# Optimization experiments

Hardware: AMD Instinct MI355X
Metric: run time of the kernel (lower is better)

Reference implementation:

```python
import jax, jax.numpy as jnp
import numpy as np

N, E, B = 50000, 800000, 64
IN_DIM, HID = 128, 64
H1 = 2  # heads in gat1
NEG_SLOPE = 0.2


def _glorot(key, shape):
    fan_in = shape[0]
    return jax.random.normal(key, shape, dtype=jnp.float32) / jnp.sqrt(jnp.float32(fan_in))


def setup_inputs() -> dict:
    key = jax.random.key(0)
    ks = jax.random.split(key, 24)
    x = jax.random.normal(ks[0], (N, IN_DIM), dtype=jnp.float32)
    edge_index = jax.random.randint(ks[1], (2, E), 0, N, dtype=jnp.int64)
    batch = jnp.sort(jax.random.randint(ks[2], (N,), 0, B, dtype=jnp.int64))
    d = {
        'x': x, 'edge_index': edge_index, 'batch': batch,
        # gat1: in=128 -> heads=2, out=64 (concat -> 128)
        'w1_l': _glorot(ks[3], (IN_DIM, H1 * HID)), 'b1_l': jnp.zeros((H1 * HID,), jnp.float32),
        'w1_r': _glorot(ks[4], (IN_DIM, H1 * HID)), 'b1_r': jnp.zeros((H1 * HID,), jnp.float32),
        'att1': _glorot(ks[5], (H1, HID)), 'bias1': jnp.zeros((H1 * HID,), jnp.float32),
        # gat2: in=128 -> heads=1, out=64
        'w2_l': _glorot(ks[6], (H1 * HID, HID)), 'b2_l': jnp.zeros((HID,), jnp.float32),
        'w2_r': _glorot(ks[7], (H1 * HID, HID)), 'b2_r': jnp.zeros((HID,), jnp.float32),
        'att2': _glorot(ks[8], (1, HID)), 'bias2': jnp.zeros((HID,), jnp.float32),
        # gate_nn: Linear(64,64) -> ReLU -> Linear(64,1)
        'gate_w1': _glorot(ks[9], (HID, HID)), 'gate_b1': jnp.zeros((HID,), jnp.float32),
        'gate_w2': _glorot(ks[10], (HID, 1)), 'gate_b2': jnp.zeros((1,), jnp.float32),
        # MLP head
        'lin1_w': _glorot(ks[11], (HID, HID)), 'lin1_b': jnp.zeros((HID,), jnp.float32),
        'lin2_w': _glorot(ks[12], (HID, 1)), 'lin2_b': jnp.zeros((1,), jnp.float32),
    }
    return d


def _segment_softmax(scores, seg, num_segments):
    # scores: [E, H]; softmax over edges sharing the same seg id (per column)
    m = jax.ops.segment_max(scores, seg, num_segments=num_segments)
    m = jnp.where(jnp.isfinite(m), m, 0.0)
    ex = jnp.exp(scores - m[seg])
    s = jax.ops.segment_sum(ex, seg, num_segments=num_segments)
    return ex / (s[seg] + 1e-16)


def _gatv2(x, src, dst, w_l, b_l, w_r, b_r, att, bias, heads, out_dim, n_nodes):
    xl = (x @ w_l + b_l).reshape(n_nodes, heads, out_dim)
    xr = (x @ w_r + b_r).reshape(n_nodes, heads, out_dim)
    e = jax.nn.leaky_relu(xl[src] + xr[dst], NEG_SLOPE)      # [E,H,D]
    score = jnp.einsum('ehd,hd->eh', e, att)                  # [E,H]
    alpha = _segment_softmax(score, dst, n_nodes)             # [E,H]
    out = jax.ops.segment_sum(alpha[..., None] * xl[src], dst, num_segments=n_nodes)
    return out.reshape(n_nodes, heads * out_dim) + bias


def reference(x, edge_index, batch, w1_l, b1_l, w1_r, b1_r, att1, bias1,
              w2_l, b2_l, w2_r, b2_r, att2, bias2,
              gate_w1, gate_b1, gate_w2, gate_b2,
              lin1_w, lin1_b, lin2_w, lin2_b):
    n = x.shape[0]
    # PyG GATv2Conv default add_self_loops=True
    loop = jnp.arange(n, dtype=edge_index.dtype)
    src = jnp.concatenate([edge_index[0], loop])
    dst = jnp.concatenate([edge_index[1], loop])

    h = jax.nn.relu(_gatv2(x, src, dst, w1_l, b1_l, w1_r, b1_r, att1, bias1, H1, HID, n))
    h = jax.nn.relu(_gatv2(h, src, dst, w2_l, b2_l, w2_r, b2_r, att2, bias2, 1, HID, n))

    # GlobalAttention pool: gate = gate_nn(h); softmax over batch; weighted sum
    gate = jax.nn.relu(h @ gate_w1 + gate_b1) @ gate_w2 + gate_b2     # [N,1]
    alpha = _segment_softmax(gate, batch, B)                           # [N,1]
    pooled = jax.ops.segment_sum(alpha * h, batch, num_segments=B)     # [B,HID]

    out = jax.nn.relu(pooled @ lin1_w + lin1_b)
    out = (out @ lin2_w + lin2_b).squeeze(-1)                          # [B]
    return out
```

## Files before the change

### kernel.cpp

```cpp
#include <hip/hip_runtime.h>

typedef float v2f __attribute__((ext_vector_type(2)));
typedef float v4f __attribute__((ext_vector_type(4)));
typedef _Float16 h4 __attribute__((ext_vector_type(4)));

template<int N> struct IC { static constexpr int value = N; };


__global__ void k_init(const float* __restrict__ w1_l, const float* __restrict__ w1_r,
                       const float* __restrict__ b1_l, const float* __restrict__ b1_r,
                       const float* __restrict__ w2_l, const float* __restrict__ w2_r,
                       const float* __restrict__ b2_l, const float* __restrict__ b2_r,
                       float* __restrict__ wc1, float* __restrict__ bc1,
                       float* __restrict__ wc2, float* __restrict__ bc2,
                       int* __restrict__ deg, int n){
  int i = blockIdx.x*256 + threadIdx.x;
  if (i < n) deg[i] = 0;
  if (i < 128*256){
    int k = i >> 8, j = i & 255;
    wc1[i] = (j < 128) ? w1_l[k*128 + j] : w1_r[k*128 + (j - 128)];
  }
  if (i < 128*128){
    int k = i >> 7, j = i & 127;
    wc2[i] = (j < 64) ? w2_l[k*64 + j] : w2_r[k*64 + (j - 64)];
  }
  if (i < 256) bc1[i] = (i < 128) ? b1_l[i] : b1_r[i - 128];
  if (i < 128) bc2[i] = (i < 64)  ? b2_l[i] : b2_r[i - 64];
}

__global__ void k_hist(const int* __restrict__ dstp, int* __restrict__ deg, int E){
  int e = blockIdx.x*256 + threadIdx.x;
  if (e < E) atomicAdd(&deg[dstp[e]], 1);
}

__global__ void k_scan1(const int* __restrict__ deg, int* __restrict__ rowptr,
                        int* __restrict__ bsum, int n){
  __shared__ int s[256];
  int i = blockIdx.x*256 + threadIdx.x;
  int v = (i < n) ? deg[i] + 1 : 0;
  s[threadIdx.x] = v;
  __syncthreads();
  for (int off = 1; off < 256; off <<= 1){
    int t = (threadIdx.x >= off) ? s[threadIdx.x - off] : 0;
    __syncthreads();
    s[threadIdx.x] += t;
    __syncthreads();
  }
  if (i < n) rowptr[i] = s[threadIdx.x] - v;
  if (threadIdx.x == 255) bsum[blockIdx.x] = s[255];
}

__global__ void k_scan2(int* bsum, int nb){
  __shared__ int s[256];
  int v = (threadIdx.x < nb) ? bsum[threadIdx.x] : 0;
  s[threadIdx.x] = v;
  __syncthreads();
  for (int off = 1; off < 256; off <<= 1){
    int t = (threadIdx.x >= off) ? s[threadIdx.x - off] : 0;
    __syncthreads();
    s[threadIdx.x] += t;
    __syncthreads();
  }
  if (threadIdx.x < nb) bsum[threadIdx.x] = s[threadIdx.x] - v;
}

__global__ void k_scan3(int* rowptr, const int* __restrict__ bsum,
                        int* __restrict__ srcs, int* __restrict__ cursor,
                        int n, int total){
  int i = blockIdx.x*256 + threadIdx.x;
  if (i < n){
    int b = rowptr[i] + bsum[blockIdx.x];
    rowptr[i] = b;
    srcs[b] = i;
    cursor[i] = b + 1;
  }
  if (i == 0) rowptr[n] = total;
}

__global__ void k_scatter(const int* __restrict__ srcp, const int* __restrict__ dstp,
                          int* __restrict__ cursor, int* __restrict__ srcs, int E){
  int e = blockIdx.x*256 + threadIdx.x;
  if (e < E){
    int p = atomicAdd(&cursor[dstp[e]], 1);
    srcs[p] = srcp[e];
  }
}


#define TBM 64
#define TBN 128
#define TBK 32

__global__ __launch_bounds__(256, 4) void k_gemm64(
    const float* __restrict__ A, const float* __restrict__ W,
    const float* __restrict__ bias, _Float16* __restrict__ Cxl,
    float* __restrict__ Cxr, int M, int K, int N, int xlCols){
  __shared__ float As[TBK][TBM];
  __shared__ float Ws[TBK][TBN];
  int bm = blockIdx.x * TBM, bn = blockIdx.y * TBN;
  int tid = threadIdx.x;
  int tx = tid & 15, ty = tid >> 4;
  float acc[4][8] = {};
  for (int k0 = 0; k0 < K; k0 += TBK){
    #pragma unroll
    for (int l = 0; l < 2; l++){
      int idx = tid + l*256;
      int r = idx >> 3, kq = (idx & 7) * 4;
      float4 v = make_float4(0.f, 0.f, 0.f, 0.f);
      if (bm + r < M) v = *(const float4*)(A + (size_t)(bm + r)*K + k0 + kq);
      int rc = r ^ ((idx & 7) << 3);
      As[kq+0][rc] = v.x; As[kq+1][rc] = v.y; As[kq+2][rc] = v.z; As[kq+3][rc] = v.w;
    }
    #pragma unroll
    for (int l = 0; l < 4; l++){
      int idx = tid + l*256;
      int kr = idx >> 5, wc = (idx & 31) * 4;
      *(float4*)(&Ws[kr][wc]) = *(const float4*)(W + (size_t)(k0 + kr)*N + bn + wc);
    }
    __syncthreads();
    #pragma unroll
    for (int k = 0; k < TBK; k++){
      float a[4], w[8];
      *(float4*)(a)   = *(const float4*)(&As[k][(ty*4) ^ (((k >> 2) & 7) << 3)]);
      *(float4*)(w)   = *(const float4*)(&Ws[k][tx*4]);
      *(float4*)(w+4) = *(const float4*)(&Ws[k][64 + tx*4]);
      #pragma unroll
      for (int i = 0; i < 4; i++)
        #pragma unroll
        for (int j = 0; j < 8; j++)
          acc[i][j] = fmaf(a[i], w[j], acc[i][j]);
    }
    __syncthreads();
  }
  int NR = N - xlCols;
  #pragma unroll
  for (int i = 0; i < 4; i++){
    int r = bm + ty*4 + i;
    if (r < M){
      #pragma unroll
      for (int g = 0; g < 2; g++){
        int c = bn + g*64 + tx*4;
        float o0 = acc[i][g*4+0] + bias[c+0];
        float o1 = acc[i][g*4+1] + bias[c+1];
        float o2 = acc[i][g*4+2] + bias[c+2];
        float o3 = acc[i][g*4+3] + bias[c+3];
        if (c < xlCols){
          h4 oh = {(_Float16)o0, (_Float16)o1, (_Float16)o2, (_Float16)o3};
          *(h4*)(Cxl + (size_t)r*xlCols + c) = oh;
        } else {
          float4 of = make_float4(o0, o1, o2, o3);
          *(float4*)(Cxr + (size_t)r*NR + (c - xlCols)) = of;
        }
      }
    }
  }
}


template<int CTRL>
__device__ __forceinline__ float dpp_add(float x){
  int t = __builtin_amdgcn_update_dpp(0, __float_as_int(x), CTRL, 0xf, 0xf, true);
  return x + __int_as_float(t);
}


template<int H>
__global__ __launch_bounds__(256) void k_gat_fused(
    const _Float16* __restrict__ xlh, const float* __restrict__ xr,
    const int* __restrict__ rowptr, const int* __restrict__ srcs,
    const float* __restrict__ att, const float* __restrict__ bias,
    float* __restrict__ out, int n){
  int gid = blockIdx.x * blockDim.x + threadIdx.x;
  int nd = gid >> 6, lane = gid & 63;
  if (nd >= n) return;
  constexpr int SHIFTB = (H == 2) ? 8 : 7;
  constexpr int EPI = (H == 2) ? 2 : 4;
  const int q = lane & 15;
  const int hsel = (H == 2) ? ((lane >> 4) & 1) : 0;
  const int elane = (H == 2) ? (lane >> 5) : (lane >> 4);
  const int fpos = hsel*64 + q*4;
  const unsigned foff = (unsigned)fpos * 2u;
  const char* __restrict__ xbase = (const char*)xlh;
  v4f xrv = *(const v4f*)(xr + (size_t)nd*(H*64) + fpos);
  v4f av  = *(const v4f*)(att + fpos);
  v4f acc = {0.f, 0.f, 0.f, 0.f};
  float den = 0.f;
  int s0 = rowptr[nd], s1 = rowptr[nd+1];
  for (int base = s0; base < s1; base += 64){
    int idx = base + lane;
    int sv = (idx < s1) ? srcs[idx] : 0;
    int cnt = min(64, s1 - base);
    auto batchU = [&](int i, auto Uc, bool full){
      constexpr int U = decltype(Uc)::value;
      int aidx[U];
      h4 hv[U];
      #pragma unroll
      for (int u = 0; u < U; u++)
        aidx[u] = __builtin_amdgcn_ds_bpermute((i + u*EPI + elane) << 2, sv);
      #pragma unroll
      for (int u = 0; u < U; u++)
        hv[u] = *(const h4*)(xbase + (((unsigned)aidx[u] << SHIFTB) + foff));
      #pragma unroll
      for (int u = 0; u < U; u++){
        v4f xv = {(float)hv[u].x, (float)hv[u].y, (float)hv[u].z, (float)hv[u].w};
        v4f t  = xv + xrv;
        v4f lt = __builtin_elementwise_max(t, t * 0.2f);
        v4f pr = lt * av;
        float p = (pr.x + pr.y) + (pr.z + pr.w);
        p = dpp_add<0x111>(p);
        p = dpp_add<0x112>(p);
        p = dpp_add<0x114>(p);
        p = dpp_add<0x118>(p);
        p = __int_as_float(__builtin_amdgcn_ds_swizzle(__float_as_int(p), 0x1F0));
        float ex = __expf(p);
        if (!full) ex = (elane < cnt - (i + u*EPI)) ? ex : 0.f;
        den += ex;
        acc += xv * ex;
      }
    };
    int i = 0;
    for (; i + 8*EPI <= cnt; i += 8*EPI) batchU(i, IC<8>{}, true);
    if (i + 4*EPI <= cnt){ batchU(i, IC<4>{}, true); i += 4*EPI; }
    if (i + 2*EPI <= cnt){ batchU(i, IC<2>{}, true); i += 2*EPI; }
    for (; i < cnt; i += EPI) batchU(i, IC<1>{}, i + EPI <= cnt);
  }
  if (H == 1){
    den   += __shfl_xor(den,   16, 64);
    acc.x += __shfl_xor(acc.x, 16, 64);
    acc.y += __shfl_xor(acc.y, 16, 64);
    acc.z += __shfl_xor(acc.z, 16, 64);
    acc.w += __shfl_xor(acc.w, 16, 64);
  }
  den   += __shfl_xor(den,   32, 64);
  acc.x += __shfl_xor(acc.x, 32, 64);
  acc.y += __shfl_xor(acc.y, 32, 64);
  acc.z += __shfl_xor(acc.z, 32, 64);
  acc.w += __shfl_xor(acc.w, 32, 64);
  if (lane < 16*H){
    v4f bv = *(const v4f*)(bias + lane*4);
    float inv = 1.f / (den + 1e-16f);
    v4f o = acc * inv + bv;
    v4f z = {0.f, 0.f, 0.f, 0.f};
    o = __builtin_elementwise_max(o, z);
    *(v4f*)(out + (size_t)nd*(H*64) + lane*4) = o;
  }
}


__global__ __launch_bounds__(256) void k_gate(
    const float* __restrict__ h2, const float* __restrict__ gw1,
    const float* __restrict__ gb1, const float* __restrict__ gw2,
    const float* __restrict__ gb2, float* __restrict__ exn, int M){
  __shared__ float As[32][64 + 4];
  __shared__ float Ws[32][64];
  int bm = blockIdx.x * 64;
  int tid = threadIdx.x;
  int tx = tid & 15, ty = tid >> 4;
  float acc[4][4] = {};
  for (int k0 = 0; k0 < 64; k0 += 32){
    #pragma unroll
    for (int l = 0; l < 2; l++){
      int idx = tid + l*256;
      int r = idx >> 3, c4 = (idx & 7) * 4;
      float4 v = make_float4(0.f, 0.f, 0.f, 0.f);
      if (bm + r < M) v = *(const float4*)(h2 + (size_t)(bm + r)*64 + k0 + c4);
      As[c4+0][r] = v.x; As[c4+1][r] = v.y; As[c4+2][r] = v.z; As[c4+3][r] = v.w;
      int kr = idx >> 4, wc4 = (idx & 15) * 4;
      *(float4*)(&Ws[kr][wc4]) = *(const float4*)(gw1 + (size_t)(k0 + kr)*64 + wc4);
    }
    __syncthreads();
    #pragma unroll
    for (int k = 0; k < 32; k++){
      float4 a4 = *(const float4*)(&As[k][ty*4]);
      float4 w4 = *(const float4*)(&Ws[k][tx*4]);
      float av[4] = {a4.x, a4.y, a4.z, a4.w};
      float wv[4] = {w4.x, w4.y, w4.z, w4.w};
      #pragma unroll
      for (int i = 0; i < 4; i++)
        #pragma unroll
        for (int j = 0; j < 4; j++)
          acc[i][j] = fmaf(av[i], wv[j], acc[i][j]);
    }
    __syncthreads();
  }
  float4 b4 = *(const float4*)(gb1 + tx*4);
  float4 w2 = *(const float4*)(gw2 + tx*4);
  float gb2v = gb2[0];
  #pragma unroll
  for (int i = 0; i < 4; i++){
    float p = fmaxf(acc[i][0] + b4.x, 0.f) * w2.x;
    p = fmaf(fmaxf(acc[i][1] + b4.y, 0.f), w2.y, p);
    p = fmaf(fmaxf(acc[i][2] + b4.z, 0.f), w2.z, p);
    p = fmaf(fmaxf(acc[i][3] + b4.w, 0.f), w2.w, p);
    p = dpp_add<0x111>(p);
    p = dpp_add<0x112>(p);
    p = dpp_add<0x114>(p);
    p = dpp_add<0x118>(p);
    if (tx == 15){
      int r = bm + ty*4 + i;
      if (r < M) exn[r] = __expf(p + gb2v);
    }
  }
}


__global__ __launch_bounds__(1024) void k_pool_mlp(
    const float* __restrict__ h2, const float* __restrict__ exn,
    const int* __restrict__ batch, int n,
    const float* __restrict__ l1w, const float* __restrict__ l1b,
    const float* __restrict__ l2w, const float* __restrict__ l2b,
    float* __restrict__ out){
  __shared__ float accs[16][64];
  __shared__ float dens[16];
  int b = blockIdx.x;
  int tid = threadIdx.x, lane = tid & 63, wv = tid >> 6;
  int lo = 0, hi = n;
  while (lo < hi){ int m = (lo + hi) >> 1; if (batch[m] < b) lo = m + 1; else hi = m; }
  int start = lo;
  hi = n;
  while (lo < hi){ int m = (lo + hi) >> 1; if (batch[m] < b + 1) lo = m + 1; else hi = m; }
  int end = lo;
  float acc = 0.f, den = 0.f;
  for (int nd = start + wv; nd < end; nd += 16){
    float ex = exn[nd];
    den += ex;
    acc = fmaf(ex, h2[(size_t)nd*64 + lane], acc);
  }
  accs[wv][lane] = acc;
  if (lane == 0) dens[wv] = den;
  __syncthreads();
  if (wv == 0){
    float p = 0.f, d = 0.f;
    #pragma unroll
    for (int w = 0; w < 16; w++){ p += accs[w][lane]; d += dens[w]; }
    p = p / (d + 1e-16f);
    float t = l1b[lane];
    #pragma unroll
    for (int k = 0; k < 64; k++)
      t = fmaf(__shfl(p, k, 64), l1w[k*64 + lane], t);
    t = fmaxf(t, 0.f) * l2w[lane];
    #pragma unroll
    for (int off = 32; off; off >>= 1) t += __shfl_xor(t, off, 64);
    if (lane == 0) out[b] = t + l2b[0];
  }
}


extern "C" void kernel_launch(void* const* d_in, const int* in_sizes, int n_in,
                              void* d_out, int out_size, void* d_ws, size_t ws_size,
                              hipStream_t stream){
  const float* x    = (const float*)d_in[0];
  const int*   ei   = (const int*)  d_in[1];
  const int*   batch= (const int*)  d_in[2];
  const float* w1_l = (const float*)d_in[3];  const float* b1_l = (const float*)d_in[4];
  const float* w1_r = (const float*)d_in[5];  const float* b1_r = (const float*)d_in[6];
  const float* att1 = (const float*)d_in[7];  const float* bias1= (const float*)d_in[8];
  const float* w2_l = (const float*)d_in[9];  const float* b2_l = (const float*)d_in[10];
  const float* w2_r = (const float*)d_in[11]; const float* b2_r = (const float*)d_in[12];
  const float* att2 = (const float*)d_in[13]; const float* bias2= (const float*)d_in[14];
  const float* gw1  = (const float*)d_in[15]; const float* gb1  = (const float*)d_in[16];
  const float* gw2  = (const float*)d_in[17]; const float* gb2  = (const float*)d_in[18];
  const float* l1w  = (const float*)d_in[19]; const float* l1b  = (const float*)d_in[20];
  const float* l2w  = (const float*)d_in[21]; const float* l2b  = (const float*)d_in[22];

  const int n = in_sizes[0] / 128;
  const int E = in_sizes[1] / 2;
  const int Bb = out_size;
  const int Etot = E + n;
  const int* srcp = ei;
  const int* dstp = ei + E;

  char* wsbase = (char*)d_ws;
  size_t off = 0;
  auto alloc = [&](size_t bytes)->char*{
    char* p = wsbase + off;
    off = (off + bytes + 255) & ~(size_t)255;
    return p;
  };
  int*   deg    = (int*)  alloc((size_t)n*4);
  int*   rowptr = (int*)  alloc((size_t)(n+1)*4);
  int*   cursor = (int*)  alloc((size_t)n*4);
  int*   bsum   = (int*)  alloc(1024);
  int*   srcs   = (int*)  alloc((size_t)Etot*4);
  float* wc1    = (float*)alloc(128*256*4);
  float* bc1    = (float*)alloc(256*4);
  float* wc2    = (float*)alloc(128*128*4);
  float* bc2    = (float*)alloc(128*4);
  _Float16* xlh1 = (_Float16*)alloc((size_t)n*128*2);
  float* xr1    = (float*)alloc((size_t)n*128*4);
  float* h1     = (float*)alloc((size_t)n*128*4);
  _Float16* xlh2 = xlh1;
  float* xr2 = xr1;
  float* h2  = xr1 + (size_t)n*64;
  float* exn = h1;

  int nb = (n + 255) / 256;
  int eb = (E + 255) / 256;
  int ib = (((n > 32768) ? n : 32768) + 255) / 256;

  k_init<<<ib, 256, 0, stream>>>(w1_l, w1_r, b1_l, b1_r, w2_l, w2_r, b2_l, b2_r,
                                 wc1, bc1, wc2, bc2, deg, n);
  k_hist<<<eb, 256, 0, stream>>>(dstp, deg, E);
  k_scan1<<<nb, 256, 0, stream>>>(deg, rowptr, bsum, n);
  k_scan2<<<1, 256, 0, stream>>>(bsum, nb);
  k_scan3<<<nb, 256, 0, stream>>>(rowptr, bsum, srcs, cursor, n, Etot);
  k_scatter<<<eb, 256, 0, stream>>>(srcp, dstp, cursor, srcs, E);

  dim3 g1((n + TBM - 1)/TBM, 256/TBN);
  k_gemm64<<<g1, 256, 0, stream>>>(x, wc1, bc1, xlh1, xr1, n, 128, 256, 128);
  long long thr = (long long)n * 64;
  int gatb = (int)((thr + 255)/256);
  k_gat_fused<2><<<gatb, 256, 0, stream>>>(xlh1, xr1, rowptr, srcs, att1, bias1, h1, n);

  dim3 g2((n + TBM - 1)/TBM, 128/TBN);
  k_gemm64<<<g2, 256, 0, stream>>>(h1, wc2, bc2, xlh2, xr2, n, 128, 128, 64);
  k_gat_fused<1><<<gatb, 256, 0, stream>>>(xlh2, xr2, rowptr, srcs, att2, bias2, h2, n);

  k_gate<<<(n + 63)/64, 256, 0, stream>>>(h2, gw1, gb1, gw2, gb2, exn, n);

  k_pool_mlp<<<Bb, 1024, 0, stream>>>(h2, exn, batch, n, l1w, l1b, l2w, l2b, (float*)d_out);
}
```

Measured before the change: 372.2 us.

## Replace FP32 SIMT GEMMs with split-FP16 MFMA GEMM

Swaps the scalar FMA GEMM used for both GAT linear projections for one built on matrix-core instructions. Operands are split into high and low FP16 parts and combined with three MFMA products to stay close to FP32 accuracy. Weights are pre-split and transposed in the init kernel, and A is converted to FP16 while it is staged in LDS. The aim is to cut the GEMM's ALU cost, at the price of extra conversion work and scalar (non-vectorised) output stores.

```diff
diff --git a/kernel.cpp b/kernel.cpp
--- a/kernel.cpp
+++ b/kernel.cpp
@@ -3,6 +3,7 @@
 typedef float v2f __attribute__((ext_vector_type(2)));
 typedef float v4f __attribute__((ext_vector_type(4)));
 typedef _Float16 h4 __attribute__((ext_vector_type(4)));
+typedef _Float16 f16x8 __attribute__((ext_vector_type(8)));
 
 template<int N> struct IC { static constexpr int value = N; };
 
@@ -11,18 +12,23 @@
                        const float* __restrict__ b1_l, const float* __restrict__ b1_r,
                        const float* __restrict__ w2_l, const float* __restrict__ w2_r,
                        const float* __restrict__ b2_l, const float* __restrict__ b2_r,
-                       float* __restrict__ wc1, float* __restrict__ bc1,
-                       float* __restrict__ wc2, float* __restrict__ bc2,
+                       _Float16* __restrict__ wc1h, _Float16* __restrict__ wc1l,
+                       _Float16* __restrict__ wc2h, _Float16* __restrict__ wc2l,
+                       float* __restrict__ bc1, float* __restrict__ bc2,
                        int* __restrict__ deg, int n){
   int i = blockIdx.x*256 + threadIdx.x;
   if (i < n) deg[i] = 0;
-  if (i < 128*256){
-    int k = i >> 8, j = i & 255;
-    wc1[i] = (j < 128) ? w1_l[k*128 + j] : w1_r[k*128 + (j - 128)];
+  if (i < 256*128){
+    int col = i >> 7, k = i & 127;
+    float v = (col < 128) ? w1_l[k*128 + col] : w1_r[k*128 + (col - 128)];
+    _Float16 h = (_Float16)v;
+    wc1h[i] = h; wc1l[i] = (_Float16)(v - (float)h);
   }
   if (i < 128*128){
-    int k = i >> 7, j = i & 127;
-    wc2[i] = (j < 64) ? w2_l[k*64 + j] : w2_r[k*64 + (j - 64)];
+    int col = i >> 7, k = i & 127;
+    float v = (col < 64) ? w2_l[k*64 + col] : w2_r[k*64 + (col - 64)];
+    _Float16 h = (_Float16)v;
+    wc2h[i] = h; wc2l[i] = (_Float16)(v - (float)h);
   }
   if (i < 256) bc1[i] = (i < 128) ? b1_l[i] : b1_r[i - 128];
   if (i < 128) bc2[i] = (i < 64)  ? b2_l[i] : b2_r[i - 64];
@@ -87,70 +93,79 @@
 }
 
 
-#define TBM 64
-#define TBN 128
-#define TBK 32
-
-__global__ __launch_bounds__(256, 4) void k_gemm64(
-    const float* __restrict__ A, const float* __restrict__ W,
-    const float* __restrict__ bias, _Float16* __restrict__ Cxl,
-    float* __restrict__ Cxr, int M, int K, int N, int xlCols){
-  __shared__ float As[TBK][TBM];
-  __shared__ float Ws[TBK][TBN];
-  int bm = blockIdx.x * TBM, bn = blockIdx.y * TBN;
+#define MBM 64
+#define MBN 128
+#define MBK 32
+
+__device__ __forceinline__ int lds_idx(int row, int k){
+  return row*32 + ((((k >> 3) ^ row) & 3) << 3) + (k & 7);
+}
+
+__global__ __launch_bounds__(256) void k_gemm_mfma(
+    const float* __restrict__ A, const _Float16* __restrict__ Wh,
+    const _Float16* __restrict__ Wl, const float* __restrict__ bias,
+    _Float16* __restrict__ Cxl, float* __restrict__ Cxr,
+    int M, int K, int N, int xlCols){
+  __shared__ _Float16 Ah[MBM*MBK], Al[MBM*MBK];
+  __shared__ _Float16 Bh[MBN*MBK], Bl[MBN*MBK];
+  int bm = blockIdx.x * MBM, bn = blockIdx.y * MBN;
   int tid = threadIdx.x;
-  int tx = tid & 15, ty = tid >> 4;
-  float acc[4][8] = {};
-  for (int k0 = 0; k0 < K; k0 += TBK){
+  int lane = tid & 63, wv = tid >> 6;
+  v4f acc[8] = {};
+  const int fragoff = (lane & 15)*32 + ((((lane >> 4) ^ lane) & 3) << 3);
+  for (int k0 = 0; k0 < K; k0 += MBK){
     #pragma unroll
     for (int l = 0; l < 2; l++){
       int idx = tid + l*256;
       int r = idx >> 3, kq = (idx & 7) * 4;
       float4 v = make_float4(0.f, 0.f, 0.f, 0.f);
       if (bm + r < M) v = *(const float4*)(A + (size_t)(bm + r)*K + k0 + kq);
-      int rc = r ^ ((idx & 7) << 3);
-      As[kq+0][rc] = v.x; As[kq+1][rc] = v.y; As[kq+2][rc] = v.z; As[kq+3][rc] = v.w;
-    }
-    #pragma unroll
-    for (int l = 0; l < 4; l++){
+      _Float16 e0 = (_Float16)v.x, e1 = (_Float16)v.y,
+               e2 = (_Float16)v.z, e3 = (_Float16)v.w;
+      h4 hh = {e0, e1, e2, e3};
+      h4 ll = {(_Float16)(v.x - (float)e0), (_Float16)(v.y - (float)e1),
+               (_Float16)(v.z - (float)e2), (_Float16)(v.w - (float)e3)};
+      int o = lds_idx(r, kq);
+      *(h4*)(&Ah[o]) = hh;
+      *(h4*)(&Al[o]) = ll;
+    }
+    #pragma unroll
+    for (int l = 0; l < 2; l++){
       int idx = tid + l*256;
-      int kr = idx >> 5, wc = (idx & 31) * 4;
-      *(float4*)(&Ws[kr][wc]) = *(const float4*)(W + (size_t)(k0 + kr)*N + bn + wc);
-    }
-    __syncthreads();
-    #pragma unroll
-    for (int k = 0; k < TBK; k++){
-      float a[4], w[8];
-      *(float4*)(a)   = *(const float4*)(&As[k][(ty*4) ^ (((k >> 2) & 7) << 3)]);
-      *(float4*)(w)   = *(const float4*)(&Ws[k][tx*4]);
-      *(float4*)(w+4) = *(const float4*)(&Ws[k][64 + tx*4]);
-      #pragma unroll
-      for (int i = 0; i < 4; i++)
-        #pragma unroll
-        for (int j = 0; j < 8; j++)
-          acc[i][j] = fmaf(a[i], w[j], acc[i][j]);
-    }
-    __syncthreads();
-  }
+      int c = idx >> 2, kc = (idx & 3) * 8;
+      size_t go = (size_t)(bn + c)*K + k0 + kc;
+      int o = lds_idx(c, kc);
+      *(f16x8*)(&Bh[o]) = *(const f16x8*)(Wh + go);
+      *(f16x8*)(&Bl[o]) = *(const f16x8*)(Wl + go);
+    }
+    __syncthreads();
+    f16x8 ah = *(const f16x8*)(&Ah[wv*16*32 + fragoff]);
+    f16x8 al = *(const f16x8*)(&Al[wv*16*32 + fragoff]);
+    #pragma unroll
+    for (int t = 0; t < 8; t++){
+      f16x8 bh = *(const f16x8*)(&Bh[t*16*32 + fragoff]);
+      f16x8 bl = *(const f16x8*)(&Bl[t*16*32 + fragoff]);
+      acc[t] = __builtin_amdgcn_mfma_f32_16x16x32_f16(ah, bh, acc[t], 0, 0, 0);
+      acc[t] = __builtin_amdgcn_mfma_f32_16x16x32_f16(ah, bl, acc[t], 0, 0, 0);
+      acc[t] = __builtin_amdgcn_mfma_f32_16x16x32_f16(al, bh, acc[t], 0, 0, 0);
+    }
+    __syncthreads();
+  }
+  int rbase = bm + wv*16 + (lane >> 4)*4;
+  int cl = lane & 15;
   int NR = N - xlCols;
   #pragma unroll
-  for (int i = 0; i < 4; i++){
-    int r = bm + ty*4 + i;
-    if (r < M){
-      #pragma unroll
-      for (int g = 0; g < 2; g++){
-        int c = bn + g*64 + tx*4;
-        float o0 = acc[i][g*4+0] + bias[c+0];
-        float o1 = acc[i][g*4+1] + bias[c+1];
-        float o2 = acc[i][g*4+2] + bias[c+2];
-        float o3 = acc[i][g*4+3] + bias[c+3];
-        if (c < xlCols){
-          h4 oh = {(_Float16)o0, (_Float16)o1, (_Float16)o2, (_Float16)o3};
-          *(h4*)(Cxl + (size_t)r*xlCols + c) = oh;
-        } else {
-          float4 of = make_float4(o0, o1, o2, o3);
-          *(float4*)(Cxr + (size_t)r*NR + (c - xlCols)) = of;
-        }
+  for (int t = 0; t < 8; t++){
+    int col = bn + t*16 + cl;
+    float bv = bias[col];
+    bool isXl = (bn + t*16) < xlCols;
+    #pragma unroll
+    for (int i = 0; i < 4; i++){
+      int r = rbase + i;
+      if (r < M){
+        float o = acc[t][i] + bv;
+        if (isXl) Cxl[(size_t)r*xlCols + col] = (_Float16)o;
+        else      Cxr[(size_t)r*NR + (col - xlCols)] = o;
       }
     }
   }
@@ -382,9 +397,11 @@
   int*   cursor = (int*)  alloc((size_t)n*4);
   int*   bsum   = (int*)  alloc(1024);
   int*   srcs   = (int*)  alloc((size_t)Etot*4);
-  float* wc1    = (float*)alloc(128*256*4);
+  _Float16* wc1h = (_Float16*)alloc(256*128*2);
+  _Float16* wc1l = (_Float16*)alloc(256*128*2);
+  _Float16* wc2h = (_Float16*)alloc(128*128*2);
+  _Float16* wc2l = (_Float16*)alloc(128*128*2);
   float* bc1    = (float*)alloc(256*4);
-  float* wc2    = (float*)alloc(128*128*4);
   float* bc2    = (float*)alloc(128*4);
   _Float16* xlh1 = (_Float16*)alloc((size_t)n*128*2);
   float* xr1    = (float*)alloc((size_t)n*128*4);
@@ -399,21 +416,21 @@
   int ib = (((n > 32768) ? n : 32768) + 255) / 256;
 
   k_init<<<ib, 256, 0, stream>>>(w1_l, w1_r, b1_l, b1_r, w2_l, w2_r, b2_l, b2_r,
-                                 wc1, bc1, wc2, bc2, deg, n);
+                                 wc1h, wc1l, wc2h, wc2l, bc1, bc2, deg, n);
   k_hist<<<eb, 256, 0, stream>>>(dstp, deg, E);
   k_scan1<<<nb, 256, 0, stream>>>(deg, rowptr, bsum, n);
   k_scan2<<<1, 256, 0, stream>>>(bsum, nb);
   k_scan3<<<nb, 256, 0, stream>>>(rowptr, bsum, srcs, cursor, n, Etot);
   k_scatter<<<eb, 256, 0, stream>>>(srcp, dstp, cursor, srcs, E);
 
-  dim3 g1((n + TBM - 1)/TBM, 256/TBN);
-  k_gemm64<<<g1, 256, 0, stream>>>(x, wc1, bc1, xlh1, xr1, n, 128, 256, 128);
+  dim3 g1((n + MBM - 1)/MBM, 2);
+  k_gemm_mfma<<<g1, 256, 0, stream>>>(x, wc1h, wc1l, bc1, xlh1, xr1, n, 128, 256, 128);
   long long thr = (long long)n * 64;
   int gatb = (int)((thr + 255)/256);
   k_gat_fused<2><<<gatb, 256, 0, stream>>>(xlh1, xr1, rowptr, srcs, att1, bias1, h1, n);
 
-  dim3 g2((n + TBM - 1)/TBM, 128/TBN);
-  k_gemm64<<<g2, 256, 0, stream>>>(h1, wc2, bc2, xlh2, xr2, n, 128, 128, 64);
+  dim3 g2((n + MBM - 1)/MBM, 1);
+  k_gemm_mfma<<<g2, 256, 0, stream>>>(h1, wc2h, wc2l, bc2, xlh2, xr2, n, 128, 128, 64);
   k_gat_fused<1><<<gatb, 256, 0, stream>>>(xlh2, xr2, rowptr, srcs, att2, bias2, h2, n);
 
   k_gate<<<(n + 63)/64, 256, 0, stream>>>(h2, gw1, gb1, gw2, gb2, exn, n);
```

Measured after the change: 349.8 us. 6.0% less time.
